# Optimization experiments

Hardware: AMD Instinct MI355X
Metric: run time of the kernel (lower is better)

Reference implementation:

```python
import jax, jax.numpy as jnp
import numpy as np

B, N, HC, HH, K, D = 64, 300, 64, 64, 3, 10

def setup_inputs() -> dict:
    key = jax.random.key(0)
    ks = jax.random.split(key, 8)
    inp = {
        "z": jax.random.normal(ks[0], (B, N, HC), dtype=jnp.float32),
        "W_in": jax.random.normal(ks[1], (HH, HC), dtype=jnp.float32) / np.sqrt(HC),
        "b_in": jax.random.normal(ks[2], (HH,), dtype=jnp.float32) * 0.01,
        "W_out": jax.random.normal(ks[3], (HC * HC, HH), dtype=jnp.float32) / np.sqrt(HH),
        "b_out": jax.random.normal(ks[4], (HC * HC,), dtype=jnp.float32) * 0.01,
        "node_emb": jax.random.normal(ks[5], (N, D), dtype=jnp.float32),
        "weights_pool": jax.random.normal(ks[6], (D, K, HH, HH), dtype=jnp.float32) / np.sqrt(D * HH),
        "bias_pool": jax.random.normal(ks[7], (D, HH), dtype=jnp.float32) * 0.01,
    }
    return inp

def _agc(z, node_emb, weights_pool, bias_pool):
    n = node_emb.shape[0]
    # data-adaptive adjacency: softmax over rows of relu(E E^T)
    supports = jax.nn.softmax(jax.nn.relu(node_emb @ node_emb.T), axis=1)  # [N,N]
    support_set = [jnp.eye(n, dtype=z.dtype), supports]
    for _ in range(2, K):  # Chebyshev recursion T_k = 2A T_{k-1} - T_{k-2}
        support_set.append(2.0 * supports @ support_set[-1] - support_set[-2])
    S = jnp.stack(support_set, axis=0)  # [K,N,N]
    weights = jnp.einsum('nd,dkio->nkio', node_emb, weights_pool)  # [N,K,HH,HH]
    bias = node_emb @ bias_pool  # [N,HH]
    x_g = jnp.einsum('knm,bmc->bnkc', S, z)  # [B,N,K,HH]
    return jnp.einsum('bnki,nkio->bno', x_g, weights) + bias

def reference(z, W_in, b_in, W_out, b_out, node_emb, weights_pool, bias_pool):
    h = jax.nn.relu(z @ W_in.T + b_in)                  # [B,N,HH]
    h = _agc(h, node_emb, weights_pool, bias_pool)      # [B,N,HH]
    out = (h @ W_out.T + b_out).reshape(B, N, HC, HC)   # [B,N,HC,HC]
    return jnp.tanh(out)
```

## Files before the change

kernel.cpp:

```cpp
#include <hip/hip_runtime.h>
#include <hip/hip_bf16.h>

#define BB 64
#define NN 300
#define HH 64
#define RTOT (BB*NN)
#define KIO  (3*HH*HH)
#define JOUT (HH*HH)

typedef __attribute__((ext_vector_type(8))) _Float16 f16x8;
typedef __attribute__((ext_vector_type(4))) float floatx4;

__device__ inline float tanh_fast(float x) {
    float e = __expf(2.f * x);
    return 1.f - 2.f * __builtin_amdgcn_rcpf(e + 1.f);
}

__global__ __launch_bounds__(256) void k_pre(const float* __restrict__ E,
                                             const float* __restrict__ z,
                                             const float* __restrict__ Win,
                                             const float* __restrict__ bin,
                                             const float* __restrict__ Wout,
                                             const float* __restrict__ pool,
                                             const float* __restrict__ bpool,
                                             float* __restrict__ A,
                                             float* __restrict__ h,
                                             float* __restrict__ Wn,
                                             float* __restrict__ bN,
                                             _Float16* __restrict__ Wh) {
    __shared__ float smem[8576];
    int bid = blockIdx.x, tid = threadIdx.x;

    if (bid < 300) {
        float* sE  = smem;
        float* row = smem + 16;
        float* red = smem + 320;
        int n = bid;
        if (tid < 10) sE[tid] = E[n*10 + tid];
        __syncthreads();
        float lmax = -1e30f;
        for (int m = tid; m < NN; m += 256) {
            float s = 0.f;
            #pragma unroll
            for (int d = 0; d < 10; ++d) s += sE[d] * E[m*10 + d];
            s = fmaxf(s, 0.f);
            row[m] = s;
            lmax = fmaxf(lmax, s);
        }
        red[tid] = lmax; __syncthreads();
        for (int off = 128; off > 0; off >>= 1) {
            if (tid < off) red[tid] = fmaxf(red[tid], red[tid+off]);
            __syncthreads();
        }
        float mx = red[0]; __syncthreads();
        float lsum = 0.f;
        for (int m = tid; m < NN; m += 256) {
            float e = __expf(row[m] - mx);
            row[m] = e;
            lsum += e;
        }
        red[tid] = lsum; __syncthreads();
        for (int off = 128; off > 0; off >>= 1) {
            if (tid < off) red[tid] += red[tid+off];
            __syncthreads();
        }
        float inv = 1.f / red[0];
        for (int m = tid; m < NN; m += 256) A[n*NN + m] = row[m] * inv;
    } else if (bid < 600) {
        float* Wt = smem;
        float* zl = smem + 4352;
        int tx = tid & 15, ty = tid >> 4;
        int r0 = (bid - 300) * 64;
        for (int e = tid; e < 4096; e += 256) {
            int o = e >> 6, c = e & 63;
            Wt[c*68 + o] = Win[e];
            zl[o*66 + c] = z[(size_t)(r0 + o)*64 + c];
        }
        __syncthreads();
        float4 bo = *(const float4*)&bin[tx*4];
        float acc[4][4];
        #pragma unroll
        for (int s = 0; s < 4; ++s) { acc[s][0]=bo.x; acc[s][1]=bo.y; acc[s][2]=bo.z; acc[s][3]=bo.w; }
        const float* zr = &zl[(ty*4)*66];
        for (int c = 0; c < 64; ++c) {
            float4 w = *(const float4*)&Wt[c*68 + tx*4];
            float z0 = zr[c], z1 = zr[66+c], z2 = zr[132+c], z3 = zr[198+c];
            acc[0][0] += z0*w.x; acc[0][1] += z0*w.y; acc[0][2] += z0*w.z; acc[0][3] += z0*w.w;
            acc[1][0] += z1*w.x; acc[1][1] += z1*w.y; acc[1][2] += z1*w.z; acc[1][3] += z1*w.w;
            acc[2][0] += z2*w.x; acc[2][1] += z2*w.y; acc[2][2] += z2*w.z; acc[2][3] += z2*w.w;
            acc[3][0] += z3*w.x; acc[3][1] += z3*w.y; acc[3][2] += z3*w.z; acc[3][3] += z3*w.w;
        }
        #pragma unroll
        for (int s = 0; s < 4; ++s) {
            float4 v = make_float4(fmaxf(acc[s][0],0.f), fmaxf(acc[s][1],0.f),
                                   fmaxf(acc[s][2],0.f), fmaxf(acc[s][3],0.f));
            *(float4*)&h[(size_t)(r0 + ty*4 + s)*64 + tx*4] = v;
        }
    } else if (bid < 675) {
        int idx = (bid - 600)*256 + tid;
        int n = idx >> 6, o = idx & 63;
        float s = 0.f;
        #pragma unroll
        for (int d = 0; d < 10; ++d) s += E[n*10 + d] * bpool[d*64 + o];
        bN[idx] = s;
    } else if (bid < 1699) {
        int idx = (bid - 675)*256 + tid;
        Wh[idx] = (_Float16)Wout[idx];
    } else {
        int idx = (bid - 1699)*256 + tid;
        int n = idx / KIO, kio = idx % KIO;
        float s = 0.f;
        #pragma unroll
        for (int d = 0; d < 10; ++d) s += E[n*10 + d] * pool[d*KIO + kio];
        Wn[idx] = s;
    }
}

__global__ __launch_bounds__(256) void k_spatialA(const float* __restrict__ A,
                                                  const float* __restrict__ h,
                                                  float* __restrict__ xg1) {
    int tid = threadIdx.x;
    int c = tid & 63;
    int w = __builtin_amdgcn_readfirstlane(tid >> 6);
    int b = blockIdx.y;
    int r0 = blockIdx.x * 20 + w * 5;
    const float* S = A + (size_t)r0 * NN;
    const float* hb = h + (size_t)b * NN * 64 + c;
    float a0 = 0.f, a1 = 0.f, a2 = 0.f, a3 = 0.f, a4 = 0.f;
    for (int m = 0; m < NN; m += 4) {
        float4 s0 = *(const float4*)(S + 0*NN + m);
        float4 s1 = *(const float4*)(S + 1*NN + m);
        float4 s2 = *(const float4*)(S + 2*NN + m);
        float4 s3 = *(const float4*)(S + 3*NN + m);
        float4 s4 = *(const float4*)(S + 4*NN + m);
        float h0 = hb[(m+0)*64];
        float h1 = hb[(m+1)*64];
        float h2 = hb[(m+2)*64];
        float h3 = hb[(m+3)*64];
        a0 = fmaf(s0.x,h0,a0); a0 = fmaf(s0.y,h1,a0); a0 = fmaf(s0.z,h2,a0); a0 = fmaf(s0.w,h3,a0);
        a1 = fmaf(s1.x,h0,a1); a1 = fmaf(s1.y,h1,a1); a1 = fmaf(s1.z,h2,a1); a1 = fmaf(s1.w,h3,a1);
        a2 = fmaf(s2.x,h0,a2); a2 = fmaf(s2.y,h1,a2); a2 = fmaf(s2.z,h2,a2); a2 = fmaf(s2.w,h3,a2);
        a3 = fmaf(s3.x,h0,a3); a3 = fmaf(s3.y,h1,a3); a3 = fmaf(s3.z,h2,a3); a3 = fmaf(s3.w,h3,a3);
        a4 = fmaf(s4.x,h0,a4); a4 = fmaf(s4.y,h1,a4); a4 = fmaf(s4.z,h2,a4); a4 = fmaf(s4.w,h3,a4);
    }
    float* dst = xg1 + ((size_t)b * NN + r0) * 64 + c;
    dst[0*64] = a0; dst[1*64] = a1; dst[2*64] = a2; dst[3*64] = a3; dst[4*64] = a4;
}

__global__ __launch_bounds__(256) void k_spatialB(const float* __restrict__ A,
                                                  const float* __restrict__ xg1,
                                                  const float* __restrict__ h,
                                                  float* __restrict__ xg2) {
    int tid = threadIdx.x;
    int c = tid & 63;
    int w = __builtin_amdgcn_readfirstlane(tid >> 6);
    int b = blockIdx.y;
    int r0 = blockIdx.x * 20 + w * 5;
    const float* S = A + (size_t)r0 * NN;
    const float* xb = xg1 + (size_t)b * NN * 64 + c;
    float a0 = 0.f, a1 = 0.f, a2 = 0.f, a3 = 0.f, a4 = 0.f;
    for (int m = 0; m < NN; m += 4) {
        float4 s0 = *(const float4*)(S + 0*NN + m);
        float4 s1 = *(const float4*)(S + 1*NN + m);
        float4 s2 = *(const float4*)(S + 2*NN + m);
        float4 s3 = *(const float4*)(S + 3*NN + m);
        float4 s4 = *(const float4*)(S + 4*NN + m);
        float x0 = xb[(m+0)*64];
        float x1 = xb[(m+1)*64];
        float x2 = xb[(m+2)*64];
        float x3 = xb[(m+3)*64];
        a0 = fmaf(s0.x,x0,a0); a0 = fmaf(s0.y,x1,a0); a0 = fmaf(s0.z,x2,a0); a0 = fmaf(s0.w,x3,a0);
        a1 = fmaf(s1.x,x0,a1); a1 = fmaf(s1.y,x1,a1); a1 = fmaf(s1.z,x2,a1); a1 = fmaf(s1.w,x3,a1);
        a2 = fmaf(s2.x,x0,a2); a2 = fmaf(s2.y,x1,a2); a2 = fmaf(s2.z,x2,a2); a2 = fmaf(s2.w,x3,a2);
        a3 = fmaf(s3.x,x0,a3); a3 = fmaf(s3.y,x1,a3); a3 = fmaf(s3.z,x2,a3); a3 = fmaf(s3.w,x3,a3);
        a4 = fmaf(s4.x,x0,a4); a4 = fmaf(s4.y,x1,a4); a4 = fmaf(s4.z,x2,a4); a4 = fmaf(s4.w,x3,a4);
    }
    const float* hb = h   + ((size_t)b * NN + r0) * 64 + c;
    float*       dst = xg2 + ((size_t)b * NN + r0) * 64 + c;
    dst[0*64] = 2.f*a0 - hb[0*64];
    dst[1*64] = 2.f*a1 - hb[1*64];
    dst[2*64] = 2.f*a2 - hb[2*64];
    dst[3*64] = 2.f*a3 - hb[3*64];
    dst[4*64] = 2.f*a4 - hb[4*64];
}

__global__ __launch_bounds__(256) void k_node_mm(const float* __restrict__ h,
                                                 const float* __restrict__ xg1,
                                                 const float* __restrict__ xg2,
                                                 const float* __restrict__ Wn,
                                                 const float* __restrict__ bN,
                                                 _Float16* __restrict__ h2h) {
    __shared__ float Wnl[192*64];
    __shared__ float xgl[8][192];
    int tid = threadIdx.x;
    int o = tid & 63, ty = tid >> 6;
    int n = blockIdx.x, b0 = blockIdx.y*8;
    for (int e = tid; e < 12288; e += 256) Wnl[e] = Wn[(size_t)n*KIO + e];
    for (int e = tid; e < 8*192; e += 256) {
        int bb = e / 192, ki = e % 192;
        int k = ki >> 6, i = ki & 63;
        const float* src = (k == 0) ? h : ((k == 1) ? xg1 : xg2);
        xgl[bb][ki] = src[((b0+bb)*NN + n)*64 + i];
    }
    __syncthreads();
    float bias = bN[n*64 + o];
    for (int bb = ty; bb < 8; bb += 4) {
        float acc = bias;
        for (int ki = 0; ki < 192; ki += 4) {
            float4 x4 = *(const float4*)&xgl[bb][ki];
            float w0 = Wnl[(ki+0)*64 + o];
            float w1 = Wnl[(ki+1)*64 + o];
            float w2 = Wnl[(ki+2)*64 + o];
            float w3 = Wnl[(ki+3)*64 + o];
            acc = fmaf(x4.x, w0, acc); acc = fmaf(x4.y, w1, acc);
            acc = fmaf(x4.z, w2, acc); acc = fmaf(x4.w, w3, acc);
        }
        h2h[((b0+bb)*NN + n)*64 + o] = (_Float16)acc;
    }
}

__global__ __launch_bounds__(256) void k_out_proj_mfma(const _Float16* __restrict__ h2h,
                                                       const _Float16* __restrict__ Wh,
                                                       const float* __restrict__ bout,
                                                       float* __restrict__ out) {
    int tid  = threadIdx.x;
    int wave = tid >> 6, lane = tid & 63;
    int quad = lane >> 4, lr = lane & 15;
    int m0 = blockIdx.y*128 + (wave >> 1)*64;
    int n0 = blockIdx.x*128 + (wave & 1)*64;
    floatx4 acc[4][4] = {};
    const _Float16* Aptr = h2h + (size_t)(m0 + lr)*64 + quad*8;
    const _Float16* Bptr = Wh  + (size_t)(n0 + lr)*64 + quad*8;
    #pragma unroll
    for (int ks = 0; ks < 2; ++ks) {
        f16x8 a[4], b[4];
        #pragma unroll
        for (int f = 0; f < 4; ++f) {
            a[f] = *(const f16x8*)(Aptr + (size_t)f*16*64 + ks*32);
            b[f] = *(const f16x8*)(Bptr + (size_t)f*16*64 + ks*32);
        }
        #pragma unroll
        for (int mf = 0; mf < 4; ++mf)
            #pragma unroll
            for (int nf = 0; nf < 4; ++nf)
                acc[mf][nf] = __builtin_amdgcn_mfma_f32_16x16x32_f16(b[nf], a[mf], acc[mf][nf], 0, 0, 0);
    }
    #pragma unroll
    for (int nf = 0; nf < 4; ++nf) {
        int c0 = n0 + nf*16 + quad*4;
        float4 bj = *(const float4*)&bout[c0];
        #pragma unroll
        for (int mf = 0; mf < 4; ++mf) {
            int row = m0 + mf*16 + lr;
            floatx4 v;
            v[0] = tanh_fast(acc[mf][nf][0] + bj.x);
            v[1] = tanh_fast(acc[mf][nf][1] + bj.y);
            v[2] = tanh_fast(acc[mf][nf][2] + bj.z);
            v[3] = tanh_fast(acc[mf][nf][3] + bj.w);
            __builtin_nontemporal_store(v, (floatx4*)&out[(size_t)row*JOUT + c0]);
        }
    }
}

extern "C" void kernel_launch(void* const* d_in, const int* in_sizes, int n_in,
                              void* d_out, int out_size, void* d_ws, size_t ws_size,
                              hipStream_t stream) {
    const float* z     = (const float*)d_in[0];
    const float* Win   = (const float*)d_in[1];
    const float* bin   = (const float*)d_in[2];
    const float* Wout  = (const float*)d_in[3];
    const float* bout  = (const float*)d_in[4];
    const float* E     = (const float*)d_in[5];
    const float* pool  = (const float*)d_in[6];
    const float* bpool = (const float*)d_in[7];
    float* out = (float*)d_out;

    float* ws  = (float*)d_ws;
    float* A   = ws;
    float* Wn  = A   + 90000;
    float* bN  = Wn  + 3686400;
    float* h   = bN  + 19200;
    float* xg1 = h   + 1228800;
    float* xg2 = xg1 + 1228800;
    _Float16* h2h   = (_Float16*)(xg2 + 1228800);
    _Float16* Wouth = h2h + 1228800;

    k_pre      <<<16099, 256, 0, stream>>>(E, z, Win, bin, Wout, pool, bpool,
                                           A, h, Wn, bN, Wouth);
    k_spatialA <<<dim3(15, BB), 256, 0, stream>>>(A, h, xg1);
    k_spatialB <<<dim3(15, BB), 256, 0, stream>>>(A, xg1, h, xg2);
    k_node_mm  <<<dim3(NN, 8), 256, 0, stream>>>(h, xg1, xg2, Wn, bN, h2h);
    k_out_proj_mfma<<<dim3(JOUT/128, RTOT/128), 256, 0, stream>>>(h2h, Wouth, bout, out);
}
```

Measured before the change: 449.3 us.

## Fuse per-node weight generation into node matmul, drop Wn buffer

The per-node weight tensor Wn (300x3x64x64 floats) is no longer built in the pre-kernel and written to global memory. Instead each k_node_mm block computes its node's weights directly into shared memory from E and the weight pool. The batch tile per block grows from 8 to 32 so that generation is amortized over more rows, which leaves a 300x2 grid. The goal is to avoid writing and reading back roughly 15 MB of Wn, at the cost of redundant pool reads per block, lower parallelism and more shared memory per block.

```diff
diff --git a/kernel.cpp b/kernel.cpp
--- a/kernel.cpp
+++ b/kernel.cpp
@@ -21,11 +21,9 @@
                                              const float* __restrict__ Win,
                                              const float* __restrict__ bin,
                                              const float* __restrict__ Wout,
-                                             const float* __restrict__ pool,
                                              const float* __restrict__ bpool,
                                              float* __restrict__ A,
                                              float* __restrict__ h,
-                                             float* __restrict__ Wn,
                                              float* __restrict__ bN,
                                              _Float16* __restrict__ Wh) {
     __shared__ float smem[8576];
@@ -103,16 +101,9 @@
         #pragma unroll
         for (int d = 0; d < 10; ++d) s += E[n*10 + d] * bpool[d*64 + o];
         bN[idx] = s;
-    } else if (bid < 1699) {
+    } else {
         int idx = (bid - 675)*256 + tid;
         Wh[idx] = (_Float16)Wout[idx];
-    } else {
-        int idx = (bid - 1699)*256 + tid;
-        int n = idx / KIO, kio = idx % KIO;
-        float s = 0.f;
-        #pragma unroll
-        for (int d = 0; d < 10; ++d) s += E[n*10 + d] * pool[d*KIO + kio];
-        Wn[idx] = s;
     }
 }
 
@@ -187,24 +178,45 @@
 __global__ __launch_bounds__(256) void k_node_mm(const float* __restrict__ h,
                                                  const float* __restrict__ xg1,
                                                  const float* __restrict__ xg2,
-                                                 const float* __restrict__ Wn,
+                                                 const float* __restrict__ pool,
+                                                 const float* __restrict__ E,
                                                  const float* __restrict__ bN,
                                                  _Float16* __restrict__ h2h) {
-    __shared__ float Wnl[192*64];
-    __shared__ float xgl[8][192];
+    __shared__ float Wnl[12288];
+    __shared__ float xgl[32][192];
     int tid = threadIdx.x;
+    int n = blockIdx.x, b0 = blockIdx.y * 32;
+
+    float Ev[10];
+    #pragma unroll
+    for (int d = 0; d < 10; ++d) Ev[d] = E[n*10 + d];
+
+    const float4* p4 = (const float4*)pool;
+    for (int e4 = tid; e4 < 3072; e4 += 256) {
+        float4 acc = make_float4(0.f, 0.f, 0.f, 0.f);
+        #pragma unroll
+        for (int d = 0; d < 10; ++d) {
+            float4 pv = p4[d*3072 + e4];
+            acc.x = fmaf(Ev[d], pv.x, acc.x);
+            acc.y = fmaf(Ev[d], pv.y, acc.y);
+            acc.z = fmaf(Ev[d], pv.z, acc.z);
+            acc.w = fmaf(Ev[d], pv.w, acc.w);
+        }
+        ((float4*)Wnl)[e4] = acc;
+    }
+
+    for (int e4 = tid; e4 < 1536; e4 += 256) {
+        int gi = e4 * 4;
+        int bb = gi / 192, kb = gi % 192;
+        int k = kb >> 6, i = kb & 63;
+        const float* src = (k == 0) ? h : ((k == 1) ? xg1 : xg2);
+        *(float4*)&xgl[bb][kb] = *(const float4*)&src[((size_t)(b0 + bb)*NN + n)*64 + i];
+    }
+    __syncthreads();
+
     int o = tid & 63, ty = tid >> 6;
-    int n = blockIdx.x, b0 = blockIdx.y*8;
-    for (int e = tid; e < 12288; e += 256) Wnl[e] = Wn[(size_t)n*KIO + e];
-    for (int e = tid; e < 8*192; e += 256) {
-        int bb = e / 192, ki = e % 192;
-        int k = ki >> 6, i = ki & 63;
-        const float* src = (k == 0) ? h : ((k == 1) ? xg1 : xg2);
-        xgl[bb][ki] = src[((b0+bb)*NN + n)*64 + i];
-    }
-    __syncthreads();
     float bias = bN[n*64 + o];
-    for (int bb = ty; bb < 8; bb += 4) {
+    for (int bb = ty; bb < 32; bb += 4) {
         float acc = bias;
         for (int ki = 0; ki < 192; ki += 4) {
             float4 x4 = *(const float4*)&xgl[bb][ki];
@@ -215,7 +227,7 @@
             acc = fmaf(x4.x, w0, acc); acc = fmaf(x4.y, w1, acc);
             acc = fmaf(x4.z, w2, acc); acc = fmaf(x4.w, w3, acc);
         }
-        h2h[((b0+bb)*NN + n)*64 + o] = (_Float16)acc;
+        h2h[((size_t)(b0 + bb)*NN + n)*64 + o] = (_Float16)acc;
     }
 }
 
@@ -277,18 +289,17 @@
 
     float* ws  = (float*)d_ws;
     float* A   = ws;
-    float* Wn  = A   + 90000;
-    float* bN  = Wn  + 3686400;
+    float* bN  = A   + 90000;
     float* h   = bN  + 19200;
     float* xg1 = h   + 1228800;
     float* xg2 = xg1 + 1228800;
     _Float16* h2h   = (_Float16*)(xg2 + 1228800);
     _Float16* Wouth = h2h + 1228800;
 
-    k_pre      <<<16099, 256, 0, stream>>>(E, z, Win, bin, Wout, pool, bpool,
-                                           A, h, Wn, bN, Wouth);
+    k_pre      <<<1699, 256, 0, stream>>>(E, z, Win, bin, Wout, bpool,
+                                          A, h, bN, Wouth);
     k_spatialA <<<dim3(15, BB), 256, 0, stream>>>(A, h, xg1);
     k_spatialB <<<dim3(15, BB), 256, 0, stream>>>(A, xg1, h, xg2);
-    k_node_mm  <<<dim3(NN, 8), 256, 0, stream>>>(h, xg1, xg2, Wn, bN, h2h);
+    k_node_mm  <<<dim3(NN, 2), 256, 0, stream>>>(h, xg1, xg2, pool, E, bN, h2h);
     k_out_proj_mfma<<<dim3(JOUT/128, RTOT/128), 256, 0, stream>>>(h2h, Wouth, bout, out);
 }
```

Measured after the change: 451.7 us. Within noise of the previous version (+0.5%).
